# Performance work log

Measured on AMD Instinct MI355X. Metric: run time of the kernel, lower is better.

## Reference

```python
import jax, jax.numpy as jnp
import numpy as np

B, N, IN, OUT, H = 8, 1024, 256, 256, 4
D = OUT // H  # head_dim = 64


def setup_inputs() -> dict:
    key = jax.random.key(0)
    k1, k2, k3, k4 = jax.random.split(key, 4)
    h = jax.random.normal(k1, (B, N, IN), dtype=jnp.float32)
    # torch Linear weight: [out, in], Wh = h @ W.T
    W = jax.random.normal(k2, (H * D, IN), dtype=jnp.float32) * (1.0 / np.sqrt(IN))
    # attention vector a: [n_heads, 2*head_dim] (xavier-uniform-ish scale)
    a = jax.random.normal(k3, (H, 2 * D), dtype=jnp.float32) * 0.1
    adj_mask = jax.random.bernoulli(k4, 0.1, (B, N, N))
    # ensure every row has at least one neighbor (self-loop) to avoid all -inf rows
    adj_mask = adj_mask | jnp.eye(N, dtype=bool)[None]
    return {"h": h, "W": W, "a": a, "adj_mask": adj_mask}


def reference(h, W, a, adj_mask):
    # Wh: [B, H, N, D]
    Wh = (h @ W.T).reshape(B, N, H, D).transpose(0, 2, 1, 3)
    # Split 'a' into src/dst halves: e_ij = leaky_relu(a_src.Wh_i + a_dst.Wh_j)
    # (mathematically identical to the original concat+einsum, without the N^2*2D tensor)
    src = jnp.einsum('bhnd,hd->bhn', Wh, a[:, :D])
    dst = jnp.einsum('bhnd,hd->bhn', Wh, a[:, D:])
    e = jax.nn.leaky_relu(src[:, :, :, None] + dst[:, :, None, :], negative_slope=0.2)
    e = jnp.where(adj_mask[:, None, :, :], e, -jnp.inf)
    att = jax.nn.softmax(e, axis=-1)
    att = jnp.where(jnp.isnan(att), 0.0, att)
    # dropout in eval mode -> identity
    h_prime = jnp.einsum('bhij,bhjd->bhid', att, Wh)
    # concat=True: [B, N, H*D]
    return h_prime.transpose(0, 2, 1, 3).reshape(B, N, H * D)
```

## Files before the change

### kernel.cpp

```cpp
#include <hip/hip_runtime.h>
#include <hip/hip_bf16.h>

#define B 8
#define N 1024
#define IN 256
#define H 4
#define D 64
#define O 256
#define BN (B*N)

typedef __attribute__((ext_vector_type(4))) float f32x4;
typedef __attribute__((ext_vector_type(8))) short short8;
typedef __attribute__((ext_vector_type(4))) short short4v;

__device__ __forceinline__ short f2bf(float f){
  __hip_bfloat16 b = __float2bfloat16(f);
  return __builtin_bit_cast(short, b);
}
__device__ __forceinline__ float bf2f(short s){
  unsigned u = ((unsigned)(unsigned short)s) << 16;
  return __builtin_bit_cast(float, u);
}

#define PACK_BLOCKS 1024
#define CVT_BLOCKS  1056
#define H_ELEMS (BN*IN)
__global__ __launch_bounds__(256) void k_prep(const int* __restrict__ adj,
                                              unsigned* __restrict__ bits,
                                              const float* __restrict__ hmat,
                                              const float* __restrict__ Wmat,
                                              short* __restrict__ hbf,
                                              short* __restrict__ wbf){
  if(blockIdx.x < PACK_BLOCKS){
    int t = blockIdx.x * 256 + threadIdx.x;
    const int4* p = (const int4*)(adj + ((size_t)t << 5));
    unsigned word = 0;
    #pragma unroll
    for(int k = 0; k < 8; k++){
      int4 m = p[k];
      word |= (m.x != 0 ? 1u : 0u) << (k*4 + 0);
      word |= (m.y != 0 ? 1u : 0u) << (k*4 + 1);
      word |= (m.z != 0 ? 1u : 0u) << (k*4 + 2);
      word |= (m.w != 0 ? 1u : 0u) << (k*4 + 3);
    }
    bits[t] = word;
  } else {
    int idx = (blockIdx.x - PACK_BLOCKS) * 256 + threadIdx.x;
    int e = idx * 8;
    const float* srcp; short* dstp;
    if(e < H_ELEMS){ srcp = hmat + e; dstp = hbf + e; }
    else           { srcp = Wmat + (e - H_ELEMS); dstp = wbf + (e - H_ELEMS); }
    float4 a0 = *(const float4*)srcp;
    float4 a1 = *(const float4*)(srcp + 4);
    short8 pk;
    pk[0]=f2bf(a0.x); pk[1]=f2bf(a0.y); pk[2]=f2bf(a0.z); pk[3]=f2bf(a0.w);
    pk[4]=f2bf(a1.x); pk[5]=f2bf(a1.y); pk[6]=f2bf(a1.z); pk[7]=f2bf(a1.w);
    *(short8*)dstp = pk;
  }
}

__global__ __launch_bounds__(256) void k_wh(const short* __restrict__ hbf,
                                            const short* __restrict__ wbf,
                                            const float* __restrict__ avec,
                                            short* __restrict__ VT,
                                            float* __restrict__ src,
                                            float* __restrict__ dst){
  const int t = threadIdx.x;
  const int hh = t >> 6, lane = t & 63, quad = lane >> 4, l16 = lane & 15;
  const int mbase = blockIdx.x * 16;
  f32x4 acc[4];
  #pragma unroll
  for(int x=0;x<4;x++) acc[x] = (f32x4){0.f,0.f,0.f,0.f};
  const short* ap = hbf + (size_t)(mbase + l16) * IN + quad * 8;
  const short* bp0 = wbf + (size_t)(hh * 64 + l16) * IN + quad * 8;
  #pragma unroll
  for(int kk = 0; kk < 8; kk++){
    const int k0 = kk * 32;
    short8 A = *(const short8*)(ap + k0);
    #pragma unroll
    for(int dt=0; dt<4; dt++){
      short8 Bf = *(const short8*)(bp0 + (size_t)dt*16*IN + k0);
      acc[dt] = __builtin_amdgcn_mfma_f32_16x16x32_bf16(A, Bf, acc[dt], 0, 0, 0);
    }
  }
  const int bb = mbase >> 10;
  const int nb = (mbase & (N-1)) + quad * 4;
  const int bh = bb * H + hh;
  #pragma unroll
  for(int dt=0; dt<4; dt++){
    int d = dt*16 + l16;
    short4v pk;
    pk[0]=f2bf(acc[dt][0]); pk[1]=f2bf(acc[dt][1]);
    pk[2]=f2bf(acc[dt][2]); pk[3]=f2bf(acc[dt][3]);
    *(short4v*)(VT + (((size_t)bh * D + d) << 10) + nb) = pk;
  }
  float as[4], ad[4];
  #pragma unroll
  for(int dt=0; dt<4; dt++){
    as[dt] = avec[hh*(2*D) + dt*16 + l16];
    ad[dt] = avec[hh*(2*D) + D + dt*16 + l16];
  }
  #pragma unroll
  for(int r=0; r<4; r++){
    float s = 0.f, dd = 0.f;
    #pragma unroll
    for(int dt=0; dt<4; dt++){ s += acc[dt][r]*as[dt]; dd += acc[dt][r]*ad[dt]; }
    #pragma unroll
    for(int off=1; off<16; off<<=1){
      s  += __shfl_xor(s, off, 64);
      dd += __shfl_xor(dd, off, 64);
    }
    if(l16 == 0){
      int n = nb + r;
      src[(size_t)bh * N + n] = s;
      dst[(size_t)bh * N + n] = dd;
    }
  }
}

__global__ __launch_bounds__(256) void k_attn(const short* __restrict__ VT,
                                              const float* __restrict__ src,
                                              const float* __restrict__ dst,
                                              const unsigned* __restrict__ bits,
                                              float* __restrict__ out){
  __shared__ float dsh[N];
  const int t = threadIdx.x;
  const int wave = t >> 6, lane = t & 63, quad = lane >> 4, l16 = lane & 15;
  const int b = blockIdx.z, hh = blockIdx.y;
  const int bh = b * H + hh;
  const int i0 = blockIdx.x * 64;
  #pragma unroll
  for(int j = t; j < N; j += 256) dsh[j] = dst[(size_t)bh * N + j];
  const int i = i0 + wave * 16 + l16;
  const float si = src[(size_t)bh * N + i];
  const int4* mp = (const int4*)(bits + ((size_t)b * N + i) * 32);
  int4 mv[8];
  #pragma unroll
  for(int k=0;k<8;k++) mv[k] = mp[k];
  const unsigned* mw = (const unsigned*)mv;
  const short* vrow = VT + (((size_t)bh * D) << 10) + quad * 8;
  f32x4 acc[4];
  #pragma unroll
  for(int x=0;x<4;x++) acc[x] = (f32x4){0.f,0.f,0.f,0.f};
  float lsum = 0.f;
  __syncthreads();
  #pragma unroll
  for(int jt = 0; jt < 32; jt++){
    const int j0 = jt * 32;
    const unsigned word = mw[jt];
    float4 d0 = *(const float4*)&dsh[j0 + quad*8];
    float4 d1 = *(const float4*)&dsh[j0 + quad*8 + 4];
    float dv[8] = {d0.x,d0.y,d0.z,d0.w,d1.x,d1.y,d1.z,d1.w};
    short8 P;
    #pragma unroll
    for(int jj=0; jj<8; jj++){
      float e = si + dv[jj];
      e = fmaxf(e, 0.2f * e);
      float p = ((word >> (quad*8 + jj)) & 1u) ? __expf(e) : 0.f;
      P[jj] = f2bf(p);
      lsum += bf2f(P[jj]);
    }
    #pragma unroll
    for(int dt=0; dt<4; dt++){
      short8 Bf = *(const short8*)(vrow + (((size_t)(dt*16 + l16)) << 10) + j0);
      acc[dt] = __builtin_amdgcn_mfma_f32_16x16x32_bf16(P, Bf, acc[dt], 0, 0, 0);
    }
  }
  lsum += __shfl_xor(lsum, 16, 64);
  lsum += __shfl_xor(lsum, 32, 64);
  #pragma unroll
  for(int r=0; r<4; r++){
    float lv = __shfl(lsum, (lane & 48) + quad*4 + r, 64);
    float inv = 1.0f / lv;
    int ig = i0 + wave*16 + quad*4 + r;
    float* op = out + ((size_t)b * N + ig) * O + hh * D + l16;
    #pragma unroll
    for(int dt=0; dt<4; dt++) op[dt*16] = acc[dt][r] * inv;
  }
}

extern "C" void kernel_launch(void* const* d_in, const int* in_sizes, int n_in,
                              void* d_out, int out_size, void* d_ws, size_t ws_size,
                              hipStream_t stream) {
  const float* hmat = (const float*)d_in[0];
  const float* Wmat = (const float*)d_in[1];
  const float* avec = (const float*)d_in[2];
  const int* adj    = (const int*)d_in[3];
  float* out = (float*)d_out;
  char* ws = (char*)d_ws;
  short*    VT    = (short*)   (ws);
  short*    hbf   = (short*)   (ws + (size_t) 4*1024*1024);
  short*    wbf   = (short*)   (ws + (size_t) 8*1024*1024);
  unsigned* bits  = (unsigned*)(ws + (size_t) 9*1024*1024);
  float*    src   = (float*)   (ws + (size_t)10*1024*1024);
  float*    dst   = (float*)   (ws + (size_t)10*1024*1024 + 131072);
  k_prep<<<PACK_BLOCKS + CVT_BLOCKS, 256, 0, stream>>>(adj, bits, hmat, Wmat, hbf, wbf);
  k_wh<<<BN/16, 256, 0, stream>>>(hbf, wbf, avec, VT, src, dst);
  k_attn<<<dim3(16, H, B), 256, 0, stream>>>(VT, src, dst, bits, out);
}
```

Baseline: 139.8 us.

## Prefetch V tiles two steps ahead and compute row sums via MFMA

```diff
diff --git a/kernel.cpp b/kernel.cpp
--- a/kernel.cpp
+++ b/kernel.cpp
@@ -16,10 +16,6 @@
 __device__ __forceinline__ short f2bf(float f){
   __hip_bfloat16 b = __float2bfloat16(f);
   return __builtin_bit_cast(short, b);
-}
-__device__ __forceinline__ float bf2f(short s){
-  unsigned u = ((unsigned)(unsigned short)s) << 16;
-  return __builtin_bit_cast(float, u);
 }
 
 #define PACK_BLOCKS 1024
@@ -118,7 +114,7 @@
   }
 }
 
-__global__ __launch_bounds__(256) void k_attn(const short* __restrict__ VT,
+__global__ __launch_bounds__(256, 4) void k_attn(const short* __restrict__ VT,
                                               const float* __restrict__ src,
                                               const float* __restrict__ dst,
                                               const unsigned* __restrict__ bits,
@@ -139,13 +135,28 @@
   for(int k=0;k<8;k++) mv[k] = mp[k];
   const unsigned* mw = (const unsigned*)mv;
   const short* vrow = VT + (((size_t)bh * D) << 10) + quad * 8;
-  f32x4 acc[4];
+  short8 ones;
+  #pragma unroll
+  for(int k=0;k<8;k++) ones[k] = (short)0x3F80;
+  f32x4 acc[4], accl;
   #pragma unroll
   for(int x=0;x<4;x++) acc[x] = (f32x4){0.f,0.f,0.f,0.f};
-  float lsum = 0.f;
+  accl = (f32x4){0.f,0.f,0.f,0.f};
+  short8 buf[3][4];
+  #pragma unroll
+  for(int pre=0; pre<2; pre++)
+    #pragma unroll
+    for(int dt=0; dt<4; dt++)
+      buf[pre][dt] = *(const short8*)(vrow + (((size_t)(dt*16 + l16)) << 10) + pre*32);
   __syncthreads();
   #pragma unroll
   for(int jt = 0; jt < 32; jt++){
+    const int cur = jt % 3, nxt = (jt + 2) % 3;
+    if(jt + 2 < 32){
+      #pragma unroll
+      for(int dt=0; dt<4; dt++)
+        buf[nxt][dt] = *(const short8*)(vrow + (((size_t)(dt*16 + l16)) << 10) + (jt+2)*32);
+    }
     const int j0 = jt * 32;
     const unsigned word = mw[jt];
     float4 d0 = *(const float4*)&dsh[j0 + quad*8];
@@ -158,20 +169,15 @@
       e = fmaxf(e, 0.2f * e);
       float p = ((word >> (quad*8 + jj)) & 1u) ? __expf(e) : 0.f;
       P[jj] = f2bf(p);
-      lsum += bf2f(P[jj]);
-    }
-    #pragma unroll
-    for(int dt=0; dt<4; dt++){
-      short8 Bf = *(const short8*)(vrow + (((size_t)(dt*16 + l16)) << 10) + j0);
-      acc[dt] = __builtin_amdgcn_mfma_f32_16x16x32_bf16(P, Bf, acc[dt], 0, 0, 0);
-    }
-  }
-  lsum += __shfl_xor(lsum, 16, 64);
-  lsum += __shfl_xor(lsum, 32, 64);
+    }
+    accl = __builtin_amdgcn_mfma_f32_16x16x32_bf16(P, ones, accl, 0, 0, 0);
+    #pragma unroll
+    for(int dt=0; dt<4; dt++)
+      acc[dt] = __builtin_amdgcn_mfma_f32_16x16x32_bf16(P, buf[cur][dt], acc[dt], 0, 0, 0);
+  }
   #pragma unroll
   for(int r=0; r<4; r++){
-    float lv = __shfl(lsum, (lane & 48) + quad*4 + r, 64);
-    float inv = 1.0f / lv;
+    float inv = 1.0f / accl[r];
     int ig = i0 + wave*16 + quad*4 + r;
     float* op = out + ((size_t)b * N + ig) * O + hh * D + l16;
     #pragma unroll
```

Result: faster. 130.1 us (median of 4 runs) (-7.0%).
